# Performance work log

Measured on AMD Instinct MI355X. Metric: run time of the kernel, lower is better.

## Reference

```python
import jax, jax.numpy as jnp
import numpy as np

N = 100000
E = 800000
IN_DIM = 128
H = 4
D = 32
HD = H * D  # 128
EPS = 1e-5
NEG_SLOPE = 0.2


def setup_inputs() -> dict:
    key = jax.random.key(0)
    ks = jax.random.split(key, 12)
    feat = jax.random.normal(ks[0], (N, IN_DIM), dtype=jnp.float32)
    src = jax.random.randint(ks[1], (E,), 0, N)
    dst = jax.random.randint(ks[2], (E,), 0, N)
    s = 1.0 / np.sqrt(IN_DIM)
    W_src = jax.random.uniform(ks[3], (HD, IN_DIM), jnp.float32, -s, s)
    b_src = jax.random.uniform(ks[4], (HD,), jnp.float32, -s, s)
    attn_l = jax.random.normal(ks[5], (1, H, D), dtype=jnp.float32) * np.sqrt(2.0 / (H * D + 1)) * np.sqrt(2.0)
    attn_r = jax.random.normal(ks[6], (1, H, D), dtype=jnp.float32) * np.sqrt(2.0 / (H * D + 1)) * np.sqrt(2.0)
    W_skip = jax.random.uniform(ks[7], (HD, IN_DIM), jnp.float32, -s, s)
    b_skip = jax.random.uniform(ks[8], (HD,), jnp.float32, -s, s)
    sg = 1.0 / np.sqrt(3 * HD)
    W_gate = jax.random.uniform(ks[9], (1, 3 * HD), jnp.float32, -sg, sg)
    b_gate = jax.random.uniform(ks[10], (1,), jnp.float32, -sg, sg)
    ln_g = jnp.ones((HD,), jnp.float32)
    ln_b = jnp.zeros((HD,), jnp.float32)
    prelu_a = jnp.full((1,), 0.25, jnp.float32)
    return {"feat": feat, "src": src, "dst": dst, "W_src": W_src, "b_src": b_src,
            "attn_l": attn_l, "attn_r": attn_r, "W_skip": W_skip, "b_skip": b_skip,
            "W_gate": W_gate, "b_gate": b_gate, "ln_g": ln_g, "ln_b": ln_b,
            "prelu_a": prelu_a}


def reference(feat, src, dst, W_src, b_src, attn_l, attn_r, W_skip, b_skip,
              W_gate, b_gate, ln_g, ln_b, prelu_a):
    # node projection -> [N, H, D]
    feat_src = (feat @ W_src.T + b_src).reshape(N, H, D)
    el = jnp.sum(feat_src * attn_l, axis=-1)  # [N, H]
    er = jnp.sum(feat_src * attn_r, axis=-1)  # [N, H]
    # per-edge logits with leaky relu
    e = el[src] + er[dst]                      # [E, H]
    e = jnp.where(e >= 0, e, NEG_SLOPE * e)
    # edge softmax over incoming edges of each dst node
    emax = jax.ops.segment_max(e, dst, num_segments=N)   # [N, H]
    ex = jnp.exp(e - emax[dst])                          # [E, H]
    esum = jax.ops.segment_sum(ex, dst, num_segments=N)  # [N, H]
    a = ex / esum[dst]                                   # [E, H]
    # weighted aggregation: sum_e a_e * ft[src_e]
    m = feat_src[src] * a[:, :, None]                    # [E, H, D]
    rst = jax.ops.segment_sum(m, dst, num_segments=N).reshape(N, HD)
    # gated skip connection
    skip = feat @ W_skip.T + b_skip                      # [N, HD]
    g_in = jnp.concatenate([rst, skip, rst - skip], axis=-1)
    gate = jax.nn.sigmoid(g_in @ W_gate.T + b_gate)      # [N, 1]
    rst = gate * rst + (1.0 - gate) * skip
    # layer norm
    mu = jnp.mean(rst, axis=-1, keepdims=True)
    var = jnp.var(rst, axis=-1, keepdims=True)
    y = (rst - mu) / jnp.sqrt(var + EPS) * ln_g + ln_b
    # PReLU (single shared alpha)
    return jnp.where(y >= 0, y, prelu_a[0] * y)
```

## Files before the change

kernel.cpp:

```cpp
#include <hip/hip_runtime.h>

typedef __attribute__((ext_vector_type(8))) short short8;
typedef __attribute__((ext_vector_type(4))) float v4f;

__device__ __forceinline__ ushort f2bf(float x) {
    unsigned u = __float_as_uint(x);
    u = u + 0x7fffu + ((u >> 16) & 1u);
    return (ushort)(u >> 16);
}
__device__ __forceinline__ float bflo(unsigned u) { return __uint_as_float(u << 16); }
__device__ __forceinline__ float bfhi(unsigned u) { return __uint_as_float(u & 0xffff0000u); }

#define CPAD 16
#define SLOT 64

__global__ __launch_bounds__(256) void k_prep(
    const float* __restrict__ Wsrc, const float* __restrict__ Wskip,
    ushort* __restrict__ Wb, int* __restrict__ counts_p, int ncnt)
{
    int b = blockIdx.x;
    if (b < 128) {
        int i = b * 256 + threadIdx.x;
        float v = (i < 16384) ? Wsrc[i] : Wskip[i - 16384];
        Wb[i] = f2bf(v);
    } else {
        int i = ((b - 128) * 256 + threadIdx.x) * 4;
        if (i < ncnt) *(int4*)(counts_p + i) = make_int4(0, 0, 0, 0);
    }
}

__global__ __launch_bounds__(256, 3) void k_mega(
    const float* __restrict__ feat, const int* __restrict__ src,
    const int* __restrict__ dst, const ushort* __restrict__ Wb,
    const float* __restrict__ bsrc, const float* __restrict__ bskip,
    const float* __restrict__ attn_l, const float* __restrict__ attn_r,
    ushort* __restrict__ feat_src, ushort* __restrict__ skip_bf,
    float* __restrict__ el, float* __restrict__ er,
    int* __restrict__ counts_p, int* __restrict__ padcsr,
    int n, int E_, int neb)
{
    __shared__ float sA[4096];
    const int tid = threadIdx.x;
    const int b = blockIdx.x;

    if (b < neb) {
        int e = b * 256 + tid;
        if (e < E_) {
            int d = dst[e];
            int r = atomicAdd(&counts_p[(size_t)d * CPAD], 1);
            if (r < SLOT) padcsr[(size_t)d * SLOT + r] = src[e];
        }
        return;
    }

    const int gb = b - neb;
    const int wave = tid >> 6, lane = tid & 63;
    const int quad = lane >> 4, l16 = lane & 15;
    const int row0 = gb * 32;
    const int n0 = wave * 64;

    {
        int trow = tid >> 5;
        int scb  = ((tid & 31) * 16) ^ ((trow & 7) << 4);
        const char* gbase = (const char*)feat;
        #pragma unroll
        for (int i = 0; i < 4; ++i) {
            int grow = row0 + i * 8 + trow;
            if (grow > n - 1) grow = n - 1;
            const void* g = gbase + (size_t)grow * 512 + scb;
            float* lp = sA + i * 1024 + wave * 256;
            __builtin_amdgcn_global_load_lds(
                (const __attribute__((address_space(1))) void*)g,
                (__attribute__((address_space(3))) void*)lp, 16, 0, 0);
        }
    }

    const ushort* bp = Wb + (size_t)(n0 + l16) * 128 + quad * 8;
    short8 bb[4][4];
    #pragma unroll
    for (int nt = 0; nt < 4; ++nt)
        #pragma unroll
        for (int k = 0; k < 4; ++k)
            bb[nt][k] = *(const short8*)(bp + nt * 2048 + k * 32);

    __syncthreads();

    v4f acc[2][4] = {};
    const char* sAB = (const char*)sA;
    const int sw = (l16 & 7) << 4;
    #pragma unroll
    for (int k = 0; k < 4; ++k) {
        int c = quad * 32 + k * 128;
        float4 f0 = *(const float4*)(sAB + l16 * 512 + ((c     ) ^ sw));
        float4 f1 = *(const float4*)(sAB + l16 * 512 + ((c + 16) ^ sw));
        float4 g0 = *(const float4*)(sAB + (l16 + 16) * 512 + ((c     ) ^ sw));
        float4 g1 = *(const float4*)(sAB + (l16 + 16) * 512 + ((c + 16) ^ sw));
        short8 a0, a1;
        a0[0] = (short)f2bf(f0.x); a0[1] = (short)f2bf(f0.y);
        a0[2] = (short)f2bf(f0.z); a0[3] = (short)f2bf(f0.w);
        a0[4] = (short)f2bf(f1.x); a0[5] = (short)f2bf(f1.y);
        a0[6] = (short)f2bf(f1.z); a0[7] = (short)f2bf(f1.w);
        a1[0] = (short)f2bf(g0.x); a1[1] = (short)f2bf(g0.y);
        a1[2] = (short)f2bf(g0.z); a1[3] = (short)f2bf(g0.w);
        a1[4] = (short)f2bf(g1.x); a1[5] = (short)f2bf(g1.y);
        a1[6] = (short)f2bf(g1.z); a1[7] = (short)f2bf(g1.w);
        #pragma unroll
        for (int nt = 0; nt < 4; ++nt) {
            acc[0][nt] = __builtin_amdgcn_mfma_f32_16x16x32_bf16(
                bb[nt][k], a0, acc[0][nt], 0, 0, 0);
            acc[1][nt] = __builtin_amdgcn_mfma_f32_16x16x32_bf16(
                bb[nt][k], a1, acc[1][nt], 0, 0, 0);
        }
    }

    #pragma unroll
    for (int nt = 0; nt < 4; ++nt) {
        int cb = n0 + nt * 16 + quad * 4;
        const float* bpb = (n0 < 128) ? (bsrc + cb) : (bskip + (cb - 128));
        float4 bias = *(const float4*)bpb;
        #pragma unroll
        for (int mt = 0; mt < 2; ++mt) {
            acc[mt][nt][0] += bias.x;
            acc[mt][nt][1] += bias.y;
            acc[mt][nt][2] += bias.z;
            acc[mt][nt][3] += bias.w;
        }
    }

    #pragma unroll
    for (int mt = 0; mt < 2; ++mt) {
        int row = row0 + mt * 16 + l16;
        if (row < n) {
            #pragma unroll
            for (int nt = 0; nt < 4; ++nt) {
                int cb = n0 + nt * 16 + quad * 4;
                unsigned lo = (unsigned)f2bf(acc[mt][nt][0]) |
                              ((unsigned)f2bf(acc[mt][nt][1]) << 16);
                unsigned hi = (unsigned)f2bf(acc[mt][nt][2]) |
                              ((unsigned)f2bf(acc[mt][nt][3]) << 16);
                uint2 pv = make_uint2(lo, hi);
                if (n0 < 128) *(uint2*)(feat_src + (size_t)row * 128 + cb) = pv;
                else          *(uint2*)(skip_bf  + (size_t)row * 128 + (cb - 128)) = pv;
            }
        }
    }

    if (wave < 2) {
        const int hb = n0 >> 5;
        float4 al[4], ar[4];
        #pragma unroll
        for (int nt = 0; nt < 4; ++nt) {
            int cb = n0 + nt * 16 + quad * 4;
            al[nt] = *(const float4*)(attn_l + cb);
            ar[nt] = *(const float4*)(attn_r + cb);
        }
        #pragma unroll
        for (int mt = 0; mt < 2; ++mt) {
            float pl0 = 0.f, pl1 = 0.f, pr0 = 0.f, pr1 = 0.f;
            #pragma unroll
            for (int i = 0; i < 4; ++i) {
                float a0v = acc[mt][0][i], a1v = acc[mt][1][i];
                float a2v = acc[mt][2][i], a3v = acc[mt][3][i];
                const float* pal0 = (const float*)&al[0]; const float* pal1 = (const float*)&al[1];
                const float* pal2 = (const float*)&al[2]; const float* pal3 = (const float*)&al[3];
                const float* par0 = (const float*)&ar[0]; const float* par1 = (const float*)&ar[1];
                const float* par2 = (const float*)&ar[2]; const float* par3 = (const float*)&ar[3];
                pl0 = fmaf(a0v, pal0[i], fmaf(a1v, pal1[i], pl0));
                pl1 = fmaf(a2v, pal2[i], fmaf(a3v, pal3[i], pl1));
                pr0 = fmaf(a0v, par0[i], fmaf(a1v, par1[i], pr0));
                pr1 = fmaf(a2v, par2[i], fmaf(a3v, par3[i], pr1));
            }
            pl0 += __shfl_xor(pl0, 16); pl0 += __shfl_xor(pl0, 32);
            pl1 += __shfl_xor(pl1, 16); pl1 += __shfl_xor(pl1, 32);
            pr0 += __shfl_xor(pr0, 16); pr0 += __shfl_xor(pr0, 32);
            pr1 += __shfl_xor(pr1, 16); pr1 += __shfl_xor(pr1, 32);
            int row = row0 + mt * 16 + l16;
            if (lane < 16 && row < n) {
                *(float2*)(el + (size_t)row * 4 + hb) = make_float2(pl0, pl1);
                *(float2*)(er + (size_t)row * 4 + hb) = make_float2(pr0, pr1);
            }
        }
    }
}

__global__ __launch_bounds__(256) void k3_fused(
    const int* __restrict__ counts_p, const int* __restrict__ padcsr,
    const float* __restrict__ el, const float* __restrict__ er,
    const ushort* __restrict__ feat_src, const ushort* __restrict__ skip_bf,
    const float* __restrict__ Wg, const float* __restrict__ bg,
    const float* __restrict__ lng, const float* __restrict__ lnb,
    const float* __restrict__ pa, float* __restrict__ out, int n)
{
    int node = blockIdx.x * 8 + (threadIdx.x >> 5);
    if (node >= n) return;
    int l32 = threadIdx.x & 31;
    int j = l32 * 4;
    int h = l32 >> 3;

    int cnt = counts_p[(size_t)node * CPAD];
    if (cnt > SLOT) cnt = SLOT;
    int beg = node * SLOT, end = beg + cnt;
    float er_h = er[(size_t)node * 4 + h];
    const ushort* fbase = feat_src + j;

    float ac0 = 0.f, ac1 = 0.f, ac2 = 0.f, ac3 = 0.f;
    float bc0 = 0.f, bc1 = 0.f, bc2 = 0.f, bc3 = 0.f;
    float wsA = 0.f, wsB = 0.f;

    for (int p0 = beg; p0 < end; p0 += 32) {
        int pv = p0 + l32;
        int sv = padcsr[pv < end ? pv : end - 1];
        int cb = end - p0; if (cb > 32) cb = 32;
        int i = 0;
        for (; i + 1 < cb; i += 2) {
            int s0 = __shfl(sv, i, 32), s1 = __shfl(sv, i + 1, 32);
            float e0 = el[(size_t)s0 * 4 + h];
            float e1 = el[(size_t)s1 * 4 + h];
            uint2 u0 = *(const uint2*)(fbase + (size_t)s0 * 128);
            uint2 u1 = *(const uint2*)(fbase + (size_t)s1 * 128);
            float t0 = e0 + er_h, t1 = e1 + er_h;
            float w0 = __expf(t0 >= 0.f ? t0 : 0.2f * t0);
            float w1 = __expf(t1 >= 0.f ? t1 : 0.2f * t1);
            wsA += w0; wsB += w1;
            ac0 = fmaf(w0, bflo(u0.x), ac0); ac1 = fmaf(w0, bfhi(u0.x), ac1);
            ac2 = fmaf(w0, bflo(u0.y), ac2); ac3 = fmaf(w0, bfhi(u0.y), ac3);
            bc0 = fmaf(w1, bflo(u1.x), bc0); bc1 = fmaf(w1, bfhi(u1.x), bc1);
            bc2 = fmaf(w1, bflo(u1.y), bc2); bc3 = fmaf(w1, bfhi(u1.y), bc3);
        }
        if (i < cb) {
            int s = __shfl(sv, i, 32);
            float t = el[(size_t)s * 4 + h] + er_h;
            float w = __expf(t >= 0.f ? t : 0.2f * t);
            uint2 u = *(const uint2*)(fbase + (size_t)s * 128);
            wsA += w;
            ac0 = fmaf(w, bflo(u.x), ac0); ac1 = fmaf(w, bfhi(u.x), ac1);
            ac2 = fmaf(w, bflo(u.y), ac2); ac3 = fmaf(w, bfhi(u.y), ac3);
        }
    }
    float wsum = wsA + wsB;
    float inv = (wsum > 0.f) ? 1.f / wsum : 0.f;
    float r0 = (ac0 + bc0) * inv, r1 = (ac1 + bc1) * inv;
    float r2 = (ac2 + bc2) * inv, r3 = (ac3 + bc3) * inv;

    uint2 su = *(const uint2*)(skip_bf + (size_t)node * 128 + j);
    float s0 = bflo(su.x), s1 = bfhi(su.x), s2 = bflo(su.y), s3 = bfhi(su.y);

    float4 wg0 = *(const float4*)(Wg + j);
    float4 wg1 = *(const float4*)(Wg + 128 + j);
    float4 wg2 = *(const float4*)(Wg + 256 + j);
    float g = r0 * wg0.x + s0 * wg1.x + (r0 - s0) * wg2.x
            + r1 * wg0.y + s1 * wg1.y + (r1 - s1) * wg2.y
            + r2 * wg0.z + s2 * wg1.z + (r2 - s2) * wg2.z
            + r3 * wg0.w + s3 * wg1.w + (r3 - s3) * wg2.w;
    #pragma unroll
    for (int m = 1; m < 32; m <<= 1) g += __shfl_xor(g, m, 32);
    float gate = 1.f / (1.f + __expf(-(g + bg[0])));

    float x0 = gate * r0 + (1.f - gate) * s0;
    float x1 = gate * r1 + (1.f - gate) * s1;
    float x2 = gate * r2 + (1.f - gate) * s2;
    float x3 = gate * r3 + (1.f - gate) * s3;

    float sm = (x0 + x1) + (x2 + x3);
    float sq = (x0 * x0 + x1 * x1) + (x2 * x2 + x3 * x3);
    #pragma unroll
    for (int m = 1; m < 32; m <<= 1) {
        sm += __shfl_xor(sm, m, 32);
        sq += __shfl_xor(sq, m, 32);
    }
    float mu = sm * (1.f / 128.f);
    float var = sq * (1.f / 128.f) - mu * mu;
    float rs = rsqrtf(var + 1e-5f);
    float alpha = pa[0];
    float4 lg = *(const float4*)(lng + j);
    float4 lb = *(const float4*)(lnb + j);
    float y0 = (x0 - mu) * rs * lg.x + lb.x;
    float y1 = (x1 - mu) * rs * lg.y + lb.y;
    float y2 = (x2 - mu) * rs * lg.z + lb.z;
    float y3 = (x3 - mu) * rs * lg.w + lb.w;
    y0 = y0 >= 0.f ? y0 : alpha * y0;
    y1 = y1 >= 0.f ? y1 : alpha * y1;
    y2 = y2 >= 0.f ? y2 : alpha * y2;
    y3 = y3 >= 0.f ? y3 : alpha * y3;
    *(float4*)(out + (size_t)node * 128 + j) = make_float4(y0, y1, y2, y3);
}

extern "C" void kernel_launch(void* const* d_in, const int* in_sizes, int n_in,
                              void* d_out, int out_size, void* d_ws, size_t ws_size,
                              hipStream_t stream)
{
    const float* feat   = (const float*)d_in[0];
    const int*   src    = (const int*)d_in[1];
    const int*   dst    = (const int*)d_in[2];
    const float* Wsrc   = (const float*)d_in[3];
    const float* bsrc   = (const float*)d_in[4];
    const float* attn_l = (const float*)d_in[5];
    const float* attn_r = (const float*)d_in[6];
    const float* Wskip  = (const float*)d_in[7];
    const float* bskip  = (const float*)d_in[8];
    const float* Wg     = (const float*)d_in[9];
    const float* bg     = (const float*)d_in[10];
    const float* lng    = (const float*)d_in[11];
    const float* lnb    = (const float*)d_in[12];
    const float* pa     = (const float*)d_in[13];

    const int n = in_sizes[0] / 128;
    const int E = in_sizes[1];
    float* out = (float*)d_out;

    float*  el       = (float*)d_ws;
    float*  er       = el + (size_t)n * 4;
    ushort* feat_src = (ushort*)(er + (size_t)n * 4);
    ushort* skip_bf  = feat_src + (size_t)n * 128;
    ushort* Wb       = skip_bf + (size_t)n * 128;
    int*    counts_p = (int*)(Wb + 32768);
    int*    padcsr   = counts_p + (size_t)n * CPAD;

    int ncnt = n * CPAD;
    int nzb = (ncnt + 1023) / 1024;
    k_prep<<<128 + nzb, 256, 0, stream>>>(Wsrc, Wskip, Wb, counts_p, ncnt);

    int neb = (E + 255) / 256;
    int ngb = (n + 31) / 32;
    k_mega<<<neb + ngb, 256, 0, stream>>>(
        feat, src, dst, Wb, bsrc, bskip, attn_l, attn_r,
        feat_src, skip_bf, el, er, counts_p, padcsr, n, E, neb);

    k3_fused<<<(n + 7) / 8, 256, 0, stream>>>(
        counts_p, padcsr, el, er, feat_src, skip_bf, Wg, bg, lng, lnb, pa, out, n);
}
```

Measured before the change: 269.0 us.

## Split edge bucketing from GEMM and make GEMM persistent with double-buffered LDS

Edge bucketing moves into the weight-conversion prep kernel, and the counter zeroing becomes a hipMemsetAsync. The node projection GEMM becomes a persistent kernel with a fixed 512-block grid that loops over 32-row tiles. It keeps the bf16 weight fragments in registers across tiles and double-buffers feature tiles in LDS with async global-to-LDS loads and explicit vmcnt waits. This removes per-block weight reloads and overlaps loads with MFMA work, at the cost of an extra launch (memset) and no longer overlapping the edge atomics with the GEMM.

```diff
diff --git a/kernel.cpp b/kernel.cpp
--- a/kernel.cpp
+++ b/kernel.cpp
@@ -13,173 +13,187 @@
 
 #define CPAD 16
 #define SLOT 64
-
-__global__ __launch_bounds__(256) void k_prep(
+#define GGRID 512
+
+__global__ __launch_bounds__(256) void k_prepedge(
     const float* __restrict__ Wsrc, const float* __restrict__ Wskip,
-    ushort* __restrict__ Wb, int* __restrict__ counts_p, int ncnt)
+    ushort* __restrict__ Wb, const int* __restrict__ src,
+    const int* __restrict__ dst, int* __restrict__ counts_p,
+    int* __restrict__ padcsr, int E_, int neb)
 {
     int b = blockIdx.x;
-    if (b < 128) {
-        int i = b * 256 + threadIdx.x;
-        float v = (i < 16384) ? Wsrc[i] : Wskip[i - 16384];
-        Wb[i] = f2bf(v);
-    } else {
-        int i = ((b - 128) * 256 + threadIdx.x) * 4;
-        if (i < ncnt) *(int4*)(counts_p + i) = make_int4(0, 0, 0, 0);
-    }
-}
-
-__global__ __launch_bounds__(256, 3) void k_mega(
-    const float* __restrict__ feat, const int* __restrict__ src,
-    const int* __restrict__ dst, const ushort* __restrict__ Wb,
-    const float* __restrict__ bsrc, const float* __restrict__ bskip,
-    const float* __restrict__ attn_l, const float* __restrict__ attn_r,
-    ushort* __restrict__ feat_src, ushort* __restrict__ skip_bf,
-    float* __restrict__ el, float* __restrict__ er,
-    int* __restrict__ counts_p, int* __restrict__ padcsr,
-    int n, int E_, int neb)
-{
-    __shared__ float sA[4096];
-    const int tid = threadIdx.x;
-    const int b = blockIdx.x;
-
     if (b < neb) {
-        int e = b * 256 + tid;
+        int e = b * 256 + threadIdx.x;
         if (e < E_) {
             int d = dst[e];
             int r = atomicAdd(&counts_p[(size_t)d * CPAD], 1);
             if (r < SLOT) padcsr[(size_t)d * SLOT + r] = src[e];
         }
-        return;
+    } else {
+        int i = (b - neb) * 256 + threadIdx.x;
+        float v = (i < 16384) ? Wsrc[i] : Wskip[i - 16384];
+        Wb[i] = f2bf(v);
     }
-
-    const int gb = b - neb;
+}
+
+__global__ __launch_bounds__(256, 2) void k_gemm(
+    const float* __restrict__ feat, const ushort* __restrict__ Wb,
+    const float* __restrict__ bsrc, const float* __restrict__ bskip,
+    const float* __restrict__ attn_l, const float* __restrict__ attn_r,
+    ushort* __restrict__ feat_src, ushort* __restrict__ skip_bf,
+    float* __restrict__ el, float* __restrict__ er, int n)
+{
+    __shared__ float sA[8192];
+    const int tid = threadIdx.x;
     const int wave = tid >> 6, lane = tid & 63;
     const int quad = lane >> 4, l16 = lane & 15;
-    const int row0 = gb * 32;
     const int n0 = wave * 64;
-
-    {
-        int trow = tid >> 5;
-        int scb  = ((tid & 31) * 16) ^ ((trow & 7) << 4);
-        const char* gbase = (const char*)feat;
-        #pragma unroll
-        for (int i = 0; i < 4; ++i) {
-            int grow = row0 + i * 8 + trow;
-            if (grow > n - 1) grow = n - 1;
-            const void* g = gbase + (size_t)grow * 512 + scb;
-            float* lp = sA + i * 1024 + wave * 256;
-            __builtin_amdgcn_global_load_lds(
-                (const __attribute__((address_space(1))) void*)g,
-                (__attribute__((address_space(3))) void*)lp, 16, 0, 0);
-        }
-    }
+    const int ntile = (n + 31) >> 5;
 
     const ushort* bp = Wb + (size_t)(n0 + l16) * 128 + quad * 8;
     short8 bb[4][4];
     #pragma unroll
     for (int nt = 0; nt < 4; ++nt)
         #pragma unroll
-        for (int k = 0; k < 4; ++k)
+        for (int k = 0; k < 4; ++k) {
             bb[nt][k] = *(const short8*)(bp + nt * 2048 + k * 32);
-
-    __syncthreads();
-
-    v4f acc[2][4] = {};
-    const char* sAB = (const char*)sA;
-    const int sw = (l16 & 7) << 4;
-    #pragma unroll
-    for (int k = 0; k < 4; ++k) {
-        int c = quad * 32 + k * 128;
-        float4 f0 = *(const float4*)(sAB + l16 * 512 + ((c     ) ^ sw));
-        float4 f1 = *(const float4*)(sAB + l16 * 512 + ((c + 16) ^ sw));
-        float4 g0 = *(const float4*)(sAB + (l16 + 16) * 512 + ((c     ) ^ sw));
-        float4 g1 = *(const float4*)(sAB + (l16 + 16) * 512 + ((c + 16) ^ sw));
-        short8 a0, a1;
-        a0[0] = (short)f2bf(f0.x); a0[1] = (short)f2bf(f0.y);
-        a0[2] = (short)f2bf(f0.z); a0[3] = (short)f2bf(f0.w);
-        a0[4] = (short)f2bf(f1.x); a0[5] = (short)f2bf(f1.y);
-        a0[6] = (short)f2bf(f1.z); a0[7] = (short)f2bf(f1.w);
-        a1[0] = (short)f2bf(g0.x); a1[1] = (short)f2bf(g0.y);
-        a1[2] = (short)f2bf(g0.z); a1[3] = (short)f2bf(g0.w);
-        a1[4] = (short)f2bf(g1.x); a1[5] = (short)f2bf(g1.y);
-        a1[6] = (short)f2bf(g1.z); a1[7] = (short)f2bf(g1.w);
+            asm volatile("" : "+v"(bb[nt][k]));
+        }
+
+    const int trow = tid >> 5;
+    const int scb  = ((tid & 31) * 16) ^ ((trow & 7) << 4);
+    const char* gbase = (const char*)feat;
+
+    auto stage = [&](int tt, int buf) {
+        #pragma unroll
+        for (int i = 0; i < 4; ++i) {
+            int grow = tt * 32 + i * 8 + trow;
+            if (grow > n - 1) grow = n - 1;
+            const void* g = gbase + (size_t)grow * 512 + scb;
+            float* lp = sA + buf * 4096 + i * 1024 + wave * 256;
+            __builtin_amdgcn_global_load_lds(
+                (const __attribute__((address_space(1))) void*)g,
+                (__attribute__((address_space(3))) void*)lp, 16, 0, 0);
+        }
+    };
+
+    int t = blockIdx.x;
+    if (t >= ntile) return;
+    stage(t, 0);
+    int p = 0;
+    bool first = true;
+
+    for (; t < ntile; t += GGRID) {
+        int tn = t + GGRID;
+        bool pre = (tn < ntile);
+        if (pre) stage(tn, p ^ 1);
+        if (!pre)       asm volatile("s_waitcnt vmcnt(0)" ::: "memory");
+        else if (first) asm volatile("s_waitcnt vmcnt(4)" ::: "memory");
+        else            asm volatile("s_waitcnt vmcnt(8)" ::: "memory");
+        first = false;
+        __builtin_amdgcn_s_barrier();
+        __builtin_amdgcn_sched_barrier(0);
+
+        const int row0 = t * 32;
+        v4f acc[2][4] = {};
+        const char* sAB = (const char*)sA + p * 16384;
+        const int sw = (l16 & 7) << 4;
+        #pragma unroll
+        for (int k = 0; k < 4; ++k) {
+            int c = quad * 32 + k * 128;
+            float4 f0 = *(const float4*)(sAB + l16 * 512 + ((c     ) ^ sw));
+            float4 f1 = *(const float4*)(sAB + l16 * 512 + ((c + 16) ^ sw));
+            float4 g0 = *(const float4*)(sAB + (l16 + 16) * 512 + ((c     ) ^ sw));
+            float4 g1 = *(const float4*)(sAB + (l16 + 16) * 512 + ((c + 16) ^ sw));
+            short8 a0, a1;
+            a0[0] = (short)f2bf(f0.x); a0[1] = (short)f2bf(f0.y);
+            a0[2] = (short)f2bf(f0.z); a0[3] = (short)f2bf(f0.w);
+            a0[4] = (short)f2bf(f1.x); a0[5] = (short)f2bf(f1.y);
+            a0[6] = (short)f2bf(f1.z); a0[7] = (short)f2bf(f1.w);
+            a1[0] = (short)f2bf(g0.x); a1[1] = (short)f2bf(g0.y);
+            a1[2] = (short)f2bf(g0.z); a1[3] = (short)f2bf(g0.w);
+            a1[4] = (short)f2bf(g1.x); a1[5] = (short)f2bf(g1.y);
+            a1[6] = (short)f2bf(g1.z); a1[7] = (short)f2bf(g1.w);
+            #pragma unroll
+            for (int nt = 0; nt < 4; ++nt) {
+                acc[0][nt] = __builtin_amdgcn_mfma_f32_16x16x32_bf16(
+                    bb[nt][k], a0, acc[0][nt], 0, 0, 0);
+                acc[1][nt] = __builtin_amdgcn_mfma_f32_16x16x32_bf16(
+                    bb[nt][k], a1, acc[1][nt], 0, 0, 0);
+            }
+        }
+
         #pragma unroll
         for (int nt = 0; nt < 4; ++nt) {
-            acc[0][nt] = __builtin_amdgcn_mfma_f32_16x16x32_bf16(
-                bb[nt][k], a0, acc[0][nt], 0, 0, 0);
-            acc[1][nt] = __builtin_amdgcn_mfma_f32_16x16x32_bf16(
-                bb[nt][k], a1, acc[1][nt], 0, 0, 0);
-        }
-    }
-
-    #pragma unroll
-    for (int nt = 0; nt < 4; ++nt) {
-        int cb = n0 + nt * 16 + quad * 4;
-        const float* bpb = (n0 < 128) ? (bsrc + cb) : (bskip + (cb - 128));
-        float4 bias = *(const float4*)bpb;
+            int cb = n0 + nt * 16 + quad * 4;
+            const float* bpb = (n0 < 128) ? (bsrc + cb) : (bskip + (cb - 128));
+            float4 bias = *(const float4*)bpb;
+            #pragma unroll
+            for (int mt = 0; mt < 2; ++mt) {
+                acc[mt][nt][0] += bias.x;
+                acc[mt][nt][1] += bias.y;
+                acc[mt][nt][2] += bias.z;
+                acc[mt][nt][3] += bias.w;
+            }
+        }
+
         #pragma unroll
         for (int mt = 0; mt < 2; ++mt) {
-            acc[mt][nt][0] += bias.x;
-            acc[mt][nt][1] += bias.y;
-            acc[mt][nt][2] += bias.z;
-            acc[mt][nt][3] += bias.w;
-        }
-    }
-
-    #pragma unroll
-    for (int mt = 0; mt < 2; ++mt) {
-        int row = row0 + mt * 16 + l16;
-        if (row < n) {
+            int row = row0 + mt * 16 + l16;
+            if (row < n) {
+                #pragma unroll
+                for (int nt = 0; nt < 4; ++nt) {
+                    int cb = n0 + nt * 16 + quad * 4;
+                    unsigned lo = (unsigned)f2bf(acc[mt][nt][0]) |
+                                  ((unsigned)f2bf(acc[mt][nt][1]) << 16);
+                    unsigned hi = (unsigned)f2bf(acc[mt][nt][2]) |
+                                  ((unsigned)f2bf(acc[mt][nt][3]) << 16);
+                    uint2 pv = make_uint2(lo, hi);
+                    if (n0 < 128) *(uint2*)(feat_src + (size_t)row * 128 + cb) = pv;
+                    else          *(uint2*)(skip_bf  + (size_t)row * 128 + (cb - 128)) = pv;
+                }
+            }
+        }
+
+        if (wave < 2) {
+            const int hb = n0 >> 5;
+            float4 al[4], ar[4];
             #pragma unroll
             for (int nt = 0; nt < 4; ++nt) {
                 int cb = n0 + nt * 16 + quad * 4;
-                unsigned lo = (unsigned)f2bf(acc[mt][nt][0]) |
-                              ((unsigned)f2bf(acc[mt][nt][1]) << 16);
-                unsigned hi = (unsigned)f2bf(acc[mt][nt][2]) |
-                              ((unsigned)f2bf(acc[mt][nt][3]) << 16);
-                uint2 pv = make_uint2(lo, hi);
-                if (n0 < 128) *(uint2*)(feat_src + (size_t)row * 128 + cb) = pv;
-                else          *(uint2*)(skip_bf  + (size_t)row * 128 + (cb - 128)) = pv;
-            }
-        }
-    }
-
-    if (wave < 2) {
-        const int hb = n0 >> 5;
-        float4 al[4], ar[4];
-        #pragma unroll
-        for (int nt = 0; nt < 4; ++nt) {
-            int cb = n0 + nt * 16 + quad * 4;
-            al[nt] = *(const float4*)(attn_l + cb);
-            ar[nt] = *(const float4*)(attn_r + cb);
-        }
-        #pragma unroll
-        for (int mt = 0; mt < 2; ++mt) {
-            float pl0 = 0.f, pl1 = 0.f, pr0 = 0.f, pr1 = 0.f;
+                al[nt] = *(const float4*)(attn_l + cb);
+                ar[nt] = *(const float4*)(attn_r + cb);
+            }
             #pragma unroll
-            for (int i = 0; i < 4; ++i) {
-                float a0v = acc[mt][0][i], a1v = acc[mt][1][i];
-                float a2v = acc[mt][2][i], a3v = acc[mt][3][i];
-                const float* pal0 = (const float*)&al[0]; const float* pal1 = (const float*)&al[1];
-                const float* pal2 = (const float*)&al[2]; const float* pal3 = (const float*)&al[3];
-                const float* par0 = (const float*)&ar[0]; const float* par1 = (const float*)&ar[1];
-                const float* par2 = (const float*)&ar[2]; const float* par3 = (const float*)&ar[3];
-                pl0 = fmaf(a0v, pal0[i], fmaf(a1v, pal1[i], pl0));
-                pl1 = fmaf(a2v, pal2[i], fmaf(a3v, pal3[i], pl1));
-                pr0 = fmaf(a0v, par0[i], fmaf(a1v, par1[i], pr0));
-                pr1 = fmaf(a2v, par2[i], fmaf(a3v, par3[i], pr1));
-            }
-            pl0 += __shfl_xor(pl0, 16); pl0 += __shfl_xor(pl0, 32);
-            pl1 += __shfl_xor(pl1, 16); pl1 += __shfl_xor(pl1, 32);
-            pr0 += __shfl_xor(pr0, 16); pr0 += __shfl_xor(pr0, 32);
-            pr1 += __shfl_xor(pr1, 16); pr1 += __shfl_xor(pr1, 32);
-            int row = row0 + mt * 16 + l16;
-            if (lane < 16 && row < n) {
-                *(float2*)(el + (size_t)row * 4 + hb) = make_float2(pl0, pl1);
-                *(float2*)(er + (size_t)row * 4 + hb) = make_float2(pr0, pr1);
-            }
-        }
+            for (int mt = 0; mt < 2; ++mt) {
+                float pl0 = 0.f, pl1 = 0.f, pr0 = 0.f, pr1 = 0.f;
+                #pragma unroll
+                for (int i = 0; i < 4; ++i) {
+                    float a0v = acc[mt][0][i], a1v = acc[mt][1][i];
+                    float a2v = acc[mt][2][i], a3v = acc[mt][3][i];
+                    const float* pal0 = (const float*)&al[0]; const float* pal1 = (const float*)&al[1];
+                    const float* pal2 = (const float*)&al[2]; const float* pal3 = (const float*)&al[3];
+                    const float* par0 = (const float*)&ar[0]; const float* par1 = (const float*)&ar[1];
+                    const float* par2 = (const float*)&ar[2]; const float* par3 = (const float*)&ar[3];
+                    pl0 = fmaf(a0v, pal0[i], fmaf(a1v, pal1[i], pl0));
+                    pl1 = fmaf(a2v, pal2[i], fmaf(a3v, pal3[i], pl1));
+                    pr0 = fmaf(a0v, par0[i], fmaf(a1v, par1[i], pr0));
+                    pr1 = fmaf(a2v, par2[i], fmaf(a3v, par3[i], pr1));
+                }
+                pl0 += __shfl_xor(pl0, 16); pl0 += __shfl_xor(pl0, 32);
+                pl1 += __shfl_xor(pl1, 16); pl1 += __shfl_xor(pl1, 32);
+                pr0 += __shfl_xor(pr0, 16); pr0 += __shfl_xor(pr0, 32);
+                pr1 += __shfl_xor(pr1, 16); pr1 += __shfl_xor(pr1, 32);
+                int row = row0 + mt * 16 + l16;
+                if (lane < 16 && row < n) {
+                    *(float2*)(el + (size_t)row * 4 + hb) = make_float2(pl0, pl1);
+                    *(float2*)(er + (size_t)row * 4 + hb) = make_float2(pr0, pr1);
+                }
+            }
+        }
+
+        __builtin_amdgcn_s_barrier();
+        p ^= 1;
     }
 }
 
@@ -316,15 +330,14 @@
     int*    counts_p = (int*)(Wb + 32768);
     int*    padcsr   = counts_p + (size_t)n * CPAD;
 
-    int ncnt = n * CPAD;
-    int nzb = (ncnt + 1023) / 1024;
-    k_prep<<<128 + nzb, 256, 0, stream>>>(Wsrc, Wskip, Wb, counts_p, ncnt);
+    hipMemsetAsync(counts_p, 0, (size_t)n * CPAD * sizeof(int), stream);
 
     int neb = (E + 255) / 256;
-    int ngb = (n + 31) / 32;
-    k_mega<<<neb + ngb, 256, 0, stream>>>(
-        feat, src, dst, Wb, bsrc, bskip, attn_l, attn_r,
-        feat_src, skip_bf, el, er, counts_p, padcsr, n, E, neb);
+    k_prepedge<<<neb + 128, 256, 0, stream>>>(
+        Wsrc, Wskip, Wb, src, dst, counts_p, padcsr, E, neb);
+
+    k_gemm<<<GGRID, 256, 0, stream>>>(
+        feat, Wb, bsrc, bskip, attn_l, attn_r, feat_src, skip_bf, el, er, n);
 
     k3_fused<<<(n + 7) / 8, 256, 0, stream>>>(
         counts_p, padcsr, el, er, feat_src, skip_bf, Wg, bg, lng, lnb, pa, out, n);
```

New measurement: 249.1 us. 1.08x faster.
